# Kernel tuning notes

Hardware: AMD Instinct MI355X
Metric: run time of the kernel (lower is better)

The kernel has to match this reference:

```python
import jax, jax.numpy as jnp
import numpy as np

L, B, E = 512, 32, 512
ENC_HID, DEC_HID = 512, 1024
H2 = 2 * ENC_HID            # bidirectional encoder output dim
OUT_DIM = 32000             # generation (trg) vocab
CPY_LEN = 60000             # copy vocab size (embedding rows / prediction cols)
SRC_V = 50000
NEG = -1e10


def setup_inputs() -> dict:
    key = jax.random.key(0)
    ks = jax.random.split(key, 20)
    s = 0.02
    f32 = jnp.float32
    return {
        "src": jax.random.randint(ks[0], (L, B), 0, SRC_V),
        "inp": jax.random.randint(ks[1], (B,), 0, CPY_LEN),
        "hidden": jax.random.normal(ks[2], (2, B, DEC_HID), f32),
        "c": jax.random.normal(ks[3], (2, B, DEC_HID), f32),
        "encoder_outputs": jax.random.normal(ks[4], (L, B, H2), f32),
        "mask": jnp.ones((B, L), jnp.int32),
        "selective_weights": jax.random.normal(ks[5], (B, L - 2), f32),
        "src_to_cpy": jax.random.randint(ks[6], (SRC_V,), 0, CPY_LEN),
        # learned parameters
        "emb": jax.random.normal(ks[7], (CPY_LEN, E), f32) * s,
        "W_attn": jax.random.normal(ks[8], (H2 + DEC_HID, DEC_HID), f32) * s,
        "b_attn": jnp.zeros((DEC_HID,), f32),
        "v_attn": jax.random.normal(ks[9], (DEC_HID,), f32) * s,
        "W_ih0": jax.random.normal(ks[10], (4 * DEC_HID, 2 * H2 + E), f32) * s,
        "W_hh0": jax.random.normal(ks[11], (4 * DEC_HID, DEC_HID), f32) * s,
        "b_ih0": jnp.zeros((4 * DEC_HID,), f32),
        "b_hh0": jnp.zeros((4 * DEC_HID,), f32),
        "W_ih1": jax.random.normal(ks[12], (4 * DEC_HID, DEC_HID), f32) * s,
        "W_hh1": jax.random.normal(ks[13], (4 * DEC_HID, DEC_HID), f32) * s,
        "b_ih1": jnp.zeros((4 * DEC_HID,), f32),
        "b_hh1": jnp.zeros((4 * DEC_HID,), f32),
        "W_fc": jax.random.normal(ks[14], (OUT_DIM, H2 + DEC_HID + E), f32) * s,
        "b_fc": jnp.zeros((OUT_DIM,), f32),
        "W_copy": jax.random.normal(ks[15], (DEC_HID, H2), f32) * s,
        "b_copy": jnp.zeros((DEC_HID,), f32),
    }


def _lstm_cell(x, h, c, W_ih, W_hh, b_ih, b_hh):
    # PyTorch gate order: i, f, g, o
    g = x @ W_ih.T + h @ W_hh.T + b_ih + b_hh
    i, f, gg, o = jnp.split(g, 4, axis=-1)
    c_new = jax.nn.sigmoid(f) * c + jax.nn.sigmoid(i) * jnp.tanh(gg)
    h_new = jax.nn.sigmoid(o) * jnp.tanh(c_new)
    return h_new, c_new


def reference(src, inp, hidden, c, encoder_outputs, mask, selective_weights,
              src_to_cpy, emb, W_attn, b_attn, v_attn,
              W_ih0, W_hh0, b_ih0, b_hh0, W_ih1, W_hh1, b_ih1, b_hh1,
              W_fc, b_fc, W_copy, b_copy):
    Bn = encoder_outputs.shape[1]
    Ln = encoder_outputs.shape[0]
    # update_selective_weights: mask where converted src token != prev prediction, softmax
    conv_src = src_to_cpy[src[1:-1]]              # [L-2, B]
    copy_mask = (conv_src == inp[None, :]).T      # [B, L-2]
    sel = jnp.where(copy_mask, selective_weights, NEG)
    sel = jax.nn.softmax(sel, axis=1)             # [B, L-2]
    embedded = emb[inp]                           # [B, E] (dropout in eval mode = identity)
    enc = jnp.transpose(encoder_outputs, (1, 0, 2))  # [B, L, H2]
    # Bahdanau attention over encoder outputs
    h_top = hidden[-1]                            # [B, D]
    h_rep = jnp.broadcast_to(h_top[:, None, :], (Bn, Ln, h_top.shape[-1]))
    energy = jnp.tanh(jnp.concatenate([h_rep, enc], axis=2) @ W_attn + b_attn)  # [B, L, D]
    scores = energy @ v_attn                      # [B, L]
    scores = jnp.where(mask == 0, NEG, scores)
    attn_w = jax.nn.softmax(scores, axis=1)
    attentive_read = jnp.einsum('bl,blh->bh', attn_w, enc)        # [B, H2]
    sel = jnp.where(mask[:, 1:-1] == 0, NEG, sel)                 # faithful second mask
    selective_read = jnp.einsum('bl,blh->bh', sel, enc[:, 1:-1])  # [B, H2]
    # 2-layer LSTM, single step
    x = jnp.concatenate([embedded, attentive_read, selective_read], axis=1)
    h0, c0 = _lstm_cell(x, hidden[0], c[0], W_ih0, W_hh0, b_ih0, b_hh0)
    h1, c1 = _lstm_cell(h0, hidden[1], c[1], W_ih1, W_hh1, b_ih1, b_hh1)
    hidden_new = jnp.stack([h0, h1])
    c_new = jnp.stack([c0, c1])
    # generation scores
    gen = jnp.concatenate([h1, attentive_read, embedded], axis=1) @ W_fc.T + b_fc  # [B, OUT_DIM]
    # copy scores over trimmed source positions
    proj = jnp.tanh(enc[:, 1:-1] @ W_copy.T + b_copy)             # [B, L-2, D]
    copy_scores = jnp.einsum('bld,bd->bl', proj, h1)              # [B, L-2]
    copy_scores = jnp.where(mask[:, 1:-1] == 0, NEG, copy_scores)
    # assemble predictions: generation slice + indexed scatter of copy scores
    src_cpy = src_to_cpy[src.T[:, 1:-1]]                          # [B, L-2]
    preds = jnp.zeros((Bn, CPY_LEN), gen.dtype)
    preds = preds.at[:, :OUT_DIM].set(gen)
    preds = preds.at[jnp.arange(Bn)[:, None], src_cpy].set(copy_scores)
    return preds, hidden_new, c_new, attn_w, copy_scores
```

## Files before the change

kernel.cpp:

```cpp
#include <hip/hip_runtime.h>
#include <stdint.h>

typedef unsigned short u16;
typedef unsigned int   u32;
typedef __attribute__((ext_vector_type(8))) short short8;
typedef __attribute__((ext_vector_type(4))) float f32x4;

#define NEGF (-1.0e10f)

static constexpr int LL = 512, BB = 32, EE = 512, H2 = 1024, DH = 1024;
static constexpr int KX = 2560, OUTD = 32000, CPY = 60000;

static constexpr size_t HID_OFF   = 1920000;
static constexpr size_t C_OFF     = HID_OFF + 65536;
static constexpr size_t ATTN_OFF  = C_OFF + 65536;
static constexpr size_t CS_OFF    = ATTN_OFF + 16384;

static constexpr size_t WS_ENC    = 0;
static constexpr size_t WS_WA1T   = 33554432;
static constexpr size_t WS_WA2T   = 35651584;
static constexpr size_t WS_WCT    = 37748736;
static constexpr size_t WS_HPF    = 39845888;
static constexpr size_t WS_SCORES = 39976960;
static constexpr size_t WS_CSACC  = 40042496;
static constexpr size_t WS_SELP   = 40108032;
static constexpr size_t WS_XBF    = 40173568;
static constexpr size_t WS_GENBF  = 40337408;
static constexpr size_t WS_H0PBF  = 40501248;
static constexpr size_t WS_H1PBF  = 40566784;
static constexpr size_t WS_H0NBF  = 40632320;
static constexpr size_t WS_H1     = 41222144;
static constexpr size_t WS_TOTAL  = 41353216;
static constexpr size_t WS_GPART  = WS_WA1T;
static constexpr size_t WS_TAG    = WS_ENC;

__device__ __forceinline__ u16 f2bf(float x){
  u32 u = __builtin_bit_cast(u32, x);
  u32 r = (u + 0x7FFFu + ((u >> 16) & 1u)) >> 16;
  return (u16)r;
}
__device__ __forceinline__ float bf2f(u16 h){
  u32 u = ((u32)h) << 16; return __builtin_bit_cast(float, u);
}
__device__ __forceinline__ float fsig(float x){ return 1.f/(1.f + __expf(-x)); }
__device__ __forceinline__ float ftanh(float x){
  float e = __expf(2.f*x);
  return 1.f - 2.f/(e + 1.f);
}

#define GLDS16(gp, lp) __builtin_amdgcn_global_load_lds( \
    (__attribute__((address_space(1))) void*)(gp), \
    (__attribute__((address_space(3))) void*)(lp), 16, 0, 0)

__global__ void k_f32_to_bf16(const float* __restrict__ in, u16* __restrict__ out, int n4){
  int stride = gridDim.x * blockDim.x;
  for (int i = blockIdx.x*blockDim.x + threadIdx.x; i < n4; i += stride){
    float4 v = ((const float4*)in)[i];
    u32 lo = (u32)f2bf(v.x) | ((u32)f2bf(v.y) << 16);
    u32 hi = (u32)f2bf(v.z) | ((u32)f2bf(v.w) << 16);
    ((uint2*)out)[i] = make_uint2(lo, hi);
  }
}

__global__ void k_wattn_t(const float* __restrict__ W, u16* __restrict__ wa1t, u16* __restrict__ wa2t){
  __shared__ float Tt[64*65];
  int n0 = blockIdx.x*64, k0 = blockIdx.y*64;
  int t = threadIdx.x;
  int nn = t & 63, kq = t >> 6;
  for (int kk = kq; kk < 64; kk += 4)
    Tt[kk*65 + nn] = W[(size_t)(k0+kk)*1024 + n0 + nn];
  __syncthreads();
  u16* dst = (k0 < 1024) ? wa1t : wa2t;
  int kbase = (k0 < 1024) ? k0 : (k0 - 1024);
  int kk2 = t & 63, nq = t >> 6;
  for (int nn2 = nq; nn2 < 64; nn2 += 4)
    dst[(size_t)(n0+nn2)*1024 + kbase + kk2] = f2bf(Tt[kk2*65 + nn2]);
}

__global__ void k_prep(const int* __restrict__ src, const int* __restrict__ inp,
                       const float* __restrict__ hidden, const float* __restrict__ selw,
                       const int* __restrict__ s2c, const float* __restrict__ emb,
                       const int* __restrict__ mask,
                       u16* __restrict__ xbf, u16* __restrict__ genbf,
                       u16* __restrict__ h0pbf, u16* __restrict__ h1pbf,
                       float* __restrict__ scores, float* __restrict__ csacc,
                       float* __restrict__ selp)
{
  int b = blockIdx.x, t = threadIdx.x;
  int ib = inp[b];
  for (int h = t; h < 512; h += 256){
    u16 e = f2bf(emb[(size_t)ib*512 + h]);
    xbf[b*2560 + h] = e;
    genbf[b*2560 + 2048 + h] = e;
  }
  for (int k = t; k < 1024; k += 256){
    h0pbf[b*1024 + k] = f2bf(hidden[b*1024 + k]);
    h1pbf[b*1024 + k] = f2bf(hidden[32768 + b*1024 + k]);
  }
  for (int l = t; l < 512; l += 256){
    scores[b*512 + l] = 0.f;
    csacc[b*512 + l] = 0.f;
  }
  __shared__ float red[256];
  float lg[2];
  #pragma unroll
  for (int i = 0; i < 2; ++i){
    int j = t + i*256;
    lg[i] = NEGF;
    if (j < 510){
      int cs = s2c[src[(j+1)*32 + b]];
      if (cs == ib) lg[i] = selw[b*510 + j];
    }
  }
  red[t] = fmaxf(lg[0], lg[1]); __syncthreads();
  for (int s = 128; s > 0; s >>= 1){ if (t < s) red[t] = fmaxf(red[t], red[t+s]); __syncthreads(); }
  float mx = red[0]; __syncthreads();
  float e0 = (t < 510)     ? __expf(lg[0] - mx) : 0.f;
  float e1 = (t+256 < 510) ? __expf(lg[1] - mx) : 0.f;
  red[t] = e0 + e1; __syncthreads();
  for (int s = 128; s > 0; s >>= 1){ if (t < s) red[t] += red[t+s]; __syncthreads(); }
  float inv = 1.f / red[0];
  #pragma unroll
  for (int i = 0; i < 2; ++i){
    int j = t + i*256;
    if (j < 510){
      float v = ((i == 0) ? e0 : e1) * inv;
      int l = j + 1;
      selp[b*512 + l] = (mask[b*512 + l] != 0) ? v : NEGF;
    }
  }
}

__launch_bounds__(256)
__global__ void k_mfma(const u16* __restrict__ A, int lda, int Mvalid,
                       const u16* __restrict__ Bmat, int ldb, int K,
                       const float* __restrict__ preadd, int spa,
                       const float* __restrict__ dotw, int sdw,
                       float* __restrict__ dotout, int Ldot, int skipedge,
                       float* __restrict__ outstore, int NT)
{
  __shared__ u16 As[2][128*32];
  __shared__ u16 Bs[2][128*32];
  int nwg = gridDim.x, bid = blockIdx.x;
  int q = nwg >> 3, r = nwg & 7, xc = bid & 7, ix = bid >> 3;
  int wg = (xc < r ? xc*(q+1) : r*(q+1) + (xc - r)*q) + ix;
  int mt = wg / NT, nt = wg % NT;
  int m0 = mt * 128, n0 = nt * 128;
  int tid = threadIdx.x, lane = tid & 63, wid = tid >> 6;
  int wm = wid >> 1, wn = wid & 1;

  f32x4 acc[4][4];
  #pragma unroll
  for (int i = 0; i < 4; ++i)
    #pragma unroll
    for (int j = 0; j < 4; ++j)
      acc[i][j] = (f32x4){0.f, 0.f, 0.f, 0.f};

  int r0 = tid >> 2,          s0 = tid & 3;
  int r1 = (tid + 256) >> 2;
  int xv0 = (r0 ^ (r0 >> 2)) & 3, xv1 = (r1 ^ (r1 >> 2)) & 3;
  int sc0 = (s0 ^ xv0) << 3,      sc1 = (s0 ^ xv1) << 3;
  int raA0 = m0 + r0; if (raA0 >= Mvalid) raA0 = Mvalid - 1;
  int raA1 = m0 + r1; if (raA1 >= Mvalid) raA1 = Mvalid - 1;
  int rbB0 = n0 + r0, rbB1 = n0 + r1;

  auto stage = [&](int k0, u16* asb, u16* bsb){
    GLDS16(A    + (size_t)raA0*lda + k0 + sc0, (char*)asb + tid*16);
    GLDS16(A    + (size_t)raA1*lda + k0 + sc1, (char*)asb + (tid+256)*16);
    GLDS16(Bmat + (size_t)rbB0*ldb + k0 + sc0, (char*)bsb + tid*16);
    GLDS16(Bmat + (size_t)rbB1*ldb + k0 + sc1, (char*)bsb + (tid+256)*16);
  };

  int KT = K >> 5;
  stage(0, As[0], Bs[0]);
  for (int kt = 0; kt < KT; ++kt){
    __syncthreads();
    if (kt + 1 < KT) stage((kt+1) << 5, As[(kt+1) & 1], Bs[(kt+1) & 1]);
    const char* ap = (const char*)As[kt & 1];
    const char* bp = (const char*)Bs[kt & 1];
    short8 af[4], bfr[4];
    #pragma unroll
    for (int mi = 0; mi < 4; ++mi){
      int rr = wm*64 + mi*16 + (lane & 15);
      int xv = (rr ^ (rr >> 2)) & 3;
      af[mi] = *(const short8*)(ap + rr*64 + (((lane >> 4) ^ xv) << 4));
    }
    #pragma unroll
    for (int nj = 0; nj < 4; ++nj){
      int rr = wn*64 + nj*16 + (lane & 15);
      int xv = (rr ^ (rr >> 2)) & 3;
      bfr[nj] = *(const short8*)(bp + rr*64 + (((lane >> 4) ^ xv) << 4));
    }
    #pragma unroll
    for (int mi = 0; mi < 4; ++mi)
      #pragma unroll
      for (int nj = 0; nj < 4; ++nj)
        acc[mi][nj] = __builtin_amdgcn_mfma_f32_16x16x32_bf16(af[mi], bfr[nj], acc[mi][nj], 0, 0, 0);
  }

  int g = lane >> 4, cn = lane & 15;
  if (outstore){
    int Nld = NT * 128;
    #pragma unroll
    for (int mi = 0; mi < 4; ++mi)
      #pragma unroll
      for (int rr2 = 0; rr2 < 4; ++rr2){
        int row = m0 + wm*64 + mi*16 + g*4 + rr2;
        if (row < Mvalid){
          #pragma unroll
          for (int nj = 0; nj < 4; ++nj){
            int n = n0 + wn*64 + nj*16 + cn;
            outstore[(size_t)row*Nld + n] = acc[mi][nj][rr2] + preadd[(size_t)(row & 31)*spa + n];
          }
        }
      }
  } else {
    #pragma unroll
    for (int mi = 0; mi < 4; ++mi)
      #pragma unroll
      for (int rr2 = 0; rr2 < 4; ++rr2){
        int row = m0 + wm*64 + mi*16 + g*4 + rr2;
        int bb = row & 31;
        float part = 0.f;
        #pragma unroll
        for (int nj = 0; nj < 4; ++nj){
          int n = n0 + wn*64 + nj*16 + cn;
          float tv = ftanh(acc[mi][nj][rr2] + preadd[(size_t)bb*spa + n]);
          part = fmaf(tv, dotw[(size_t)bb*sdw + n], part);
        }
        part += __shfl_xor(part, 1);
        part += __shfl_xor(part, 2);
        part += __shfl_xor(part, 4);
        part += __shfl_xor(part, 8);
        if (cn == 0){
          int l = row >> 5;
          if (!skipedge || (l > 0 && l < Ldot - 1))
            atomicAdd(&dotout[(size_t)bb*Ldot + l], part);
        }
      }
  }
}

__global__ void k_softmax_attn(const float* __restrict__ scores, const int* __restrict__ mask,
                               float* __restrict__ attnw){
  int b = blockIdx.x, t = threadIdx.x;
  __shared__ float red[256];
  float v0 = scores[b*512 + t];
  float v1 = scores[b*512 + 256 + t];
  if (mask[b*512 + t] == 0) v0 = NEGF;
  if (mask[b*512 + 256 + t] == 0) v1 = NEGF;
  red[t] = fmaxf(v0, v1); __syncthreads();
  for (int s = 128; s > 0; s >>= 1){ if (t < s) red[t] = fmaxf(red[t], red[t+s]); __syncthreads(); }
  float mx = red[0]; __syncthreads();
  float e0 = __expf(v0 - mx), e1 = __expf(v1 - mx);
  red[t] = e0 + e1; __syncthreads();
  for (int s = 128; s > 0; s >>= 1){ if (t < s) red[t] += red[t+s]; __syncthreads(); }
  float inv = 1.f / red[0];
  attnw[b*512 + t] = e0 * inv;
  attnw[b*512 + 256 + t] = e1 * inv;
}

__global__ void k_reads(const u16* __restrict__ encbf, const float* __restrict__ attnw,
                        const float* __restrict__ selp,
                        u16* __restrict__ xbf, u16* __restrict__ genbf){
  int b = blockIdx.y;
  int tid = threadIdx.x;
  int h = blockIdx.x*256 + (tid & 255);
  int lh = tid >> 8;
  float aa = 0.f, as = 0.f;
  int l0 = lh*256, l1 = l0 + 256;
  #pragma unroll 4
  for (int l = l0; l < l1; ++l){
    float e = bf2f(encbf[((size_t)l*32 + b)*1024 + h]);
    aa = fmaf(attnw[b*512 + l], e, aa);
    if (l >= 1 && l < 511) as = fmaf(selp[b*512 + l], e, as);
  }
  __shared__ float red[512][2];
  red[tid][0] = aa; red[tid][1] = as;
  __syncthreads();
  if (tid < 256){
    aa = red[tid][0] + red[tid+256][0];
    as = red[tid][1] + red[tid+256][1];
    u16 ab = f2bf(aa);
    xbf[b*2560 + 512 + h]    = ab;
    xbf[b*2560 + 1536 + h]   = f2bf(as);
    genbf[b*2560 + 1024 + h] = ab;
  }
}

__launch_bounds__(256)
__global__ void k_wgemm(const float* __restrict__ W1, const u16* __restrict__ xb1, int K1,
                        const float* __restrict__ W2, const u16* __restrict__ xb2, int K2,
                        const float* __restrict__ bias1, const float* __restrict__ bias2,
                        float* __restrict__ outB, int ldo, int cps)
{
  __shared__ u16 As[64*64];
  __shared__ u16 Bs[2][32*64];
  const int tid = threadIdx.x, lane = tid & 63, w = tid >> 6;
  const int o0 = blockIdx.x * 64;
  const int c1 = K1 >> 6;
  const int c0 = blockIdx.y * cps;

  f32x4 acc[2];
  acc[0] = (f32x4){0.f,0.f,0.f,0.f};
  acc[1] = (f32x4){0.f,0.f,0.f,0.f};

  const int ar = tid >> 2, akq = (tid & 3) * 16;
  const int aswz = (ar & 7) << 4;
  const int brow = tid >> 3, pslot = tid & 7;
  const int lslot = pslot ^ (brow & 7);

  float4 aA[4], aB[4];

  auto aload = [&](int c, float4* dst){
    const float* Wp; int Kp, kc;
    if (c < c1){ Wp = W1; Kp = K1; kc = c << 6; }
    else       { Wp = W2; Kp = K2; kc = (c - c1) << 6; }
    const float4* p = (const float4*)(Wp + (size_t)(o0 + ar)*Kp + kc + akq);
    dst[0] = p[0]; dst[1] = p[1]; dst[2] = p[2]; dst[3] = p[3];
  };
  auto bstage = [&](int c, u16* bsb){
    const u16* xp; int Kp, kc;
    if (c < c1){ xp = xb1; Kp = K1; kc = c << 6; }
    else       { xp = xb2; Kp = K2; kc = (c - c1) << 6; }
    GLDS16(xp + (size_t)brow*Kp + kc + lslot*8, (char*)bsb + tid*16);
  };

  auto body = [&](int c, float4* cur, float4* nxt, const u16* bsCur, u16* bsNxt, bool more){
    __syncthreads();
    if (more){ aload(c + 1, nxt); bstage(c + 1, bsNxt); }
    u32 p0 = (u32)f2bf(cur[0].x) | ((u32)f2bf(cur[0].y) << 16);
    u32 p1 = (u32)f2bf(cur[0].z) | ((u32)f2bf(cur[0].w) << 16);
    u32 p2 = (u32)f2bf(cur[1].x) | ((u32)f2bf(cur[1].y) << 16);
    u32 p3 = (u32)f2bf(cur[1].z) | ((u32)f2bf(cur[1].w) << 16);
    u32 p4 = (u32)f2bf(cur[2].x) | ((u32)f2bf(cur[2].y) << 16);
    u32 p5 = (u32)f2bf(cur[2].z) | ((u32)f2bf(cur[2].w) << 16);
    u32 p6 = (u32)f2bf(cur[3].x) | ((u32)f2bf(cur[3].y) << 16);
    u32 p7 = (u32)f2bf(cur[3].z) | ((u32)f2bf(cur[3].w) << 16);
    char* rowp = (char*)As + ar*128;
    *(uint4*)(rowp + ((akq*2)      ^ aswz)) = make_uint4(p0,p1,p2,p3);
    *(uint4*)(rowp + ((akq*2 + 16) ^ aswz)) = make_uint4(p4,p5,p6,p7);
    asm volatile("s_waitcnt lgkmcnt(0)" ::: "memory");
    __builtin_amdgcn_s_barrier();
    #pragma unroll
    for (int kk = 0; kk < 2; ++kk){
      int rrA = w*16 + (lane & 15);
      int kb  = kk*64 + ((lane >> 4) << 4);
      short8 af = *(const short8*)((const char*)As + rrA*128 + (kb ^ ((rrA & 7) << 4)));
      #pragma unroll
      for (int nj = 0; nj < 2; ++nj){
        int rrB = nj*16 + (lane & 15);
        short8 bfv = *(const short8*)((const char*)bsCur + rrB*128 + (kb ^ ((rrB & 7) << 4)));
        acc[nj] = __builtin_amdgcn_mfma_f32_16x16x32_bf16(af, bfv, acc[nj], 0, 0, 0);
      }
    }
  };

  aload(c0, aA); bstage(c0, Bs[0]);
  for (int li = 0; li < cps; li += 2){
    body(c0 + li,     aA, aB, Bs[0], Bs[1], true);
    body(c0 + li + 1, aB, aA, Bs[1], Bs[0], (li + 2) < cps);
  }

  int g = lane >> 4, cn = lane & 15;
  int ob = o0 + w*16 + g*4;
  float* outP = outB + (size_t)blockIdx.y * 32 * (size_t)ldo;
  float4 badd = make_float4(0.f,0.f,0.f,0.f);
  if (blockIdx.y == 0){
    if (bias1){ float4 t = *(const float4*)(bias1 + ob);
      badd.x += t.x; badd.y += t.y; badd.z += t.z; badd.w += t.w; }
    if (bias2){ float4 t = *(const float4*)(bias2 + ob);
      badd.x += t.x; badd.y += t.y; badd.z += t.z; badd.w += t.w; }
  }
  #pragma unroll
  for (int nj = 0; nj < 2; ++nj){
    int bcol = nj*16 + cn;
    float4 v = make_float4(acc[nj][0] + badd.x, acc[nj][1] + badd.y,
                           acc[nj][2] + badd.z, acc[nj][3] + badd.w);
    *(float4*)(outP + (size_t)bcol*ldo + ob) = v;
  }
}

__global__ void k_cell(const float* __restrict__ gpart, const float* __restrict__ c_in,
                       float* __restrict__ h_out, float* __restrict__ c_out,
                       u16* __restrict__ hbf, int hld, float* __restrict__ h_plain){
  int idx = blockIdx.x*256 + threadIdx.x;
  int b = idx >> 10, j = idx & 1023;
  float gi = 0.f, gf = 0.f, gg = 0.f, go = 0.f;
  #pragma unroll
  for (int p = 0; p < 4; ++p){
    const float* gb = gpart + (size_t)p*131072 + (size_t)b*4096;
    gi += gb[j];
    gf += gb[1024 + j];
    gg += gb[2048 + j];
    go += gb[3072 + j];
  }
  float cv = c_in[b*1024 + j];
  float cnv = fsig(gf)*cv + fsig(gi)*ftanh(gg);
  float hn  = fsig(go)*ftanh(cnv);
  c_out[b*1024 + j] = cnv;
  h_out[b*1024 + j] = hn;
  hbf[(size_t)b*hld + j] = f2bf(hn);
  if (h_plain) h_plain[b*1024 + j] = hn;
}

__global__ void k_zerotail(float* __restrict__ preds){
  int i = blockIdx.x*256 + threadIdx.x;
  if (i < 224000){
    int b = i / 7000, t = i % 7000;
    ((float4*)(preds + (size_t)b*CPY + OUTD))[t] = make_float4(0.f, 0.f, 0.f, 0.f);
  }
}

__global__ void k_cstag(const float* __restrict__ csacc, const int* __restrict__ mask,
                        const int* __restrict__ src, const int* __restrict__ s2c,
                        float* __restrict__ cs_out, int* __restrict__ tag){
  int i = blockIdx.x*256 + threadIdx.x;
  if (i < 16320){
    int b = i / 510, j = i % 510, l = j + 1;
    cs_out[b*510 + j] = (mask[b*512 + l] != 0) ? csacc[b*512 + l] : NEGF;
    tag[(size_t)b*CPY + s2c[src[(j+1)*32 + b]]] = -1;
  }
}
__global__ void k_tag_max(const int* __restrict__ src, const int* __restrict__ s2c,
                          int* __restrict__ tag){
  int i = blockIdx.x*256 + threadIdx.x;
  if (i < 16320){
    int b = i / 510, j = i % 510;
    atomicMax(&tag[(size_t)b*CPY + s2c[src[(j+1)*32 + b]]], j);
  }
}
__global__ void k_tag_write(const int* __restrict__ src, const int* __restrict__ s2c,
                            const int* __restrict__ tag, const float* __restrict__ cs,
                            float* __restrict__ preds){
  int i = blockIdx.x*256 + threadIdx.x;
  if (i < 16320){
    int b = i / 510, j = i % 510;
    int idx = s2c[src[(j+1)*32 + b]];
    if (tag[(size_t)b*CPY + idx] == j)
      preds[(size_t)b*CPY + idx] = cs[b*510 + j];
  }
}

extern "C" void kernel_launch(void* const* d_in, const int* in_sizes, int n_in,
                              void* d_out, int out_size, void* d_ws, size_t ws_size,
                              hipStream_t stream){
  const int*   src    = (const int*)  d_in[0];
  const int*   inp    = (const int*)  d_in[1];
  const float* hidden = (const float*)d_in[2];
  const float* cst    = (const float*)d_in[3];
  const float* enc    = (const float*)d_in[4];
  const int*   mask   = (const int*)  d_in[5];
  const float* selw   = (const float*)d_in[6];
  const int*   s2c    = (const int*)  d_in[7];
  const float* emb    = (const float*)d_in[8];
  const float* W_attn = (const float*)d_in[9];
  const float* b_attn = (const float*)d_in[10];
  const float* v_attn = (const float*)d_in[11];
  const float* W_ih0  = (const float*)d_in[12];
  const float* W_hh0  = (const float*)d_in[13];
  const float* b_ih0  = (const float*)d_in[14];
  const float* b_hh0  = (const float*)d_in[15];
  const float* W_ih1  = (const float*)d_in[16];
  const float* W_hh1  = (const float*)d_in[17];
  const float* b_ih1  = (const float*)d_in[18];
  const float* b_hh1  = (const float*)d_in[19];
  const float* W_fc   = (const float*)d_in[20];
  const float* b_fc   = (const float*)d_in[21];
  const float* W_copy = (const float*)d_in[22];
  const float* b_copy = (const float*)d_in[23];

  if (ws_size < WS_TOTAL) return;

  float* out = (float*)d_out;
  char*  ws  = (char*)d_ws;
  u16*   encbf  = (u16*)  (ws + WS_ENC);
  u16*   wa1t   = (u16*)  (ws + WS_WA1T);
  u16*   wa2t   = (u16*)  (ws + WS_WA2T);
  u16*   wct    = (u16*)  (ws + WS_WCT);
  float* hpf    = (float*)(ws + WS_HPF);
  float* scores = (float*)(ws + WS_SCORES);
  float* csacc  = (float*)(ws + WS_CSACC);
  float* selp   = (float*)(ws + WS_SELP);
  u16*   xbf    = (u16*)  (ws + WS_XBF);
  u16*   genbf  = (u16*)  (ws + WS_GENBF);
  u16*   h0pbf  = (u16*)  (ws + WS_H0PBF);
  u16*   h1pbf  = (u16*)  (ws + WS_H1PBF);
  u16*   h0nbf  = (u16*)  (ws + WS_H0NBF);
  float* gpart  = (float*)(ws + WS_GPART);
  float* h1     = (float*)(ws + WS_H1);
  int*   tag    = (int*)  (ws + WS_TAG);

  k_f32_to_bf16<<<2048, 256, 0, stream>>>(enc,    encbf, (LL*BB*H2)/4);
  k_f32_to_bf16<<<512,  256, 0, stream>>>(W_copy, wct,   (DH*H2)/4);
  k_wattn_t<<<dim3(16, 32), 256, 0, stream>>>(W_attn, wa1t, wa2t);
  k_prep<<<32, 256, 0, stream>>>(src, inp, hidden, selw, s2c, emb, mask,
                                 xbf, genbf, h0pbf, h1pbf, scores, csacc, selp);

  k_mfma<<<8, 256, 0, stream>>>(h1pbf, 1024, 32, wa1t, 1024, 1024,
                                b_attn, 0, nullptr, 0, nullptr, 512, 0, hpf, 8);
  k_mfma<<<1024, 256, 0, stream>>>(encbf, 1024, LL*BB, wa2t, 1024, 1024,
                                   hpf, 1024, v_attn, 0, scores, 512, 0, nullptr, 8);
  k_softmax_attn<<<32, 256, 0, stream>>>(scores, mask, out + ATTN_OFF);
  k_reads<<<dim3(4, 32), 512, 0, stream>>>(encbf, out + ATTN_OFF, selp, xbf, genbf);

  k_wgemm<<<dim3(64, 4), 256, 0, stream>>>(W_ih0, xbf, KX, W_hh0, h0pbf, DH,
                                           b_ih0, b_hh0, gpart, 4096, 14);
  k_cell<<<128, 256, 0, stream>>>(gpart, cst, out + HID_OFF, out + C_OFF,
                                  h0nbf, 1024, nullptr);
  k_wgemm<<<dim3(64, 4), 256, 0, stream>>>(W_ih1, h0nbf, DH, W_hh1, h1pbf, DH,
                                           b_ih1, b_hh1, gpart, 4096, 8);
  k_cell<<<128, 256, 0, stream>>>(gpart, cst + 32768, out + HID_OFF + 32768,
                                  out + C_OFF + 32768, genbf, 2560, h1);

  k_mfma<<<1024, 256, 0, stream>>>(encbf, 1024, LL*BB, wct, 1024, 1024,
                                   b_copy, 0, h1, 1024, csacc, 512, 1, nullptr, 8);

  k_wgemm<<<dim3(500, 1), 256, 0, stream>>>(W_fc, genbf, KX, nullptr, nullptr, 0,
                                            b_fc, nullptr, out, CPY, 40);
  k_zerotail<<<875, 256, 0, stream>>>(out);

  k_cstag   <<<64, 256, 0, stream>>>(csacc, mask, src, s2c, out + CS_OFF, tag);
  k_tag_max <<<64, 256, 0, stream>>>(src, s2c, tag);
  k_tag_write<<<64, 256, 0, stream>>>(src, s2c, tag, out + CS_OFF, out);
}
```

Before: 395.6 us.

## Fuse attention and copy GEMMs over shared encoder tiles, defer copy dot

The attention-score GEMM and the copy-projection GEMM both read the bf16 encoder matrix, so they now run in one kernel that loads each A tile once and keeps two accumulator sets. The tanh'd copy projection is written to a 32 MB bf16 workspace and dotted with h1 later in a new per-row kernel that also writes copy scores and resets tags, which removes the separate cstag pass. The LSTM gate GEMMs also get more split-K partitions, with the cell kernel summing a variable number of partials. The cost is extra write and read traffic for the projection buffer, doubled register pressure in the fused kernel, and bf16 rounding of the projection before the dot.

```diff
diff --git a/kernel.cpp b/kernel.cpp
--- a/kernel.cpp
+++ b/kernel.cpp
@@ -22,15 +22,14 @@
 static constexpr size_t WS_WCT    = 37748736;
 static constexpr size_t WS_HPF    = 39845888;
 static constexpr size_t WS_SCORES = 39976960;
-static constexpr size_t WS_CSACC  = 40042496;
 static constexpr size_t WS_SELP   = 40108032;
 static constexpr size_t WS_XBF    = 40173568;
 static constexpr size_t WS_GENBF  = 40337408;
 static constexpr size_t WS_H0PBF  = 40501248;
 static constexpr size_t WS_H1PBF  = 40566784;
 static constexpr size_t WS_H0NBF  = 40632320;
-static constexpr size_t WS_H1     = 41222144;
-static constexpr size_t WS_TOTAL  = 41353216;
+static constexpr size_t WS_PROJ   = 50331648;
+static constexpr size_t WS_TOTAL  = WS_PROJ + 33554432;
 static constexpr size_t WS_GPART  = WS_WA1T;
 static constexpr size_t WS_TAG    = WS_ENC;
 
@@ -83,8 +82,7 @@
                        const int* __restrict__ mask,
                        u16* __restrict__ xbf, u16* __restrict__ genbf,
                        u16* __restrict__ h0pbf, u16* __restrict__ h1pbf,
-                       float* __restrict__ scores, float* __restrict__ csacc,
-                       float* __restrict__ selp)
+                       float* __restrict__ scores, float* __restrict__ selp)
 {
   int b = blockIdx.x, t = threadIdx.x;
   int ib = inp[b];
@@ -97,10 +95,8 @@
     h0pbf[b*1024 + k] = f2bf(hidden[b*1024 + k]);
     h1pbf[b*1024 + k] = f2bf(hidden[32768 + b*1024 + k]);
   }
-  for (int l = t; l < 512; l += 256){
+  for (int l = t; l < 512; l += 256)
     scores[b*512 + l] = 0.f;
-    csacc[b*512 + l] = 0.f;
-  }
   __shared__ float red[256];
   float lg[2];
   #pragma unroll
@@ -135,15 +131,11 @@
 __global__ void k_mfma(const u16* __restrict__ A, int lda, int Mvalid,
                        const u16* __restrict__ Bmat, int ldb, int K,
                        const float* __restrict__ preadd, int spa,
-                       const float* __restrict__ dotw, int sdw,
-                       float* __restrict__ dotout, int Ldot, int skipedge,
                        float* __restrict__ outstore, int NT)
 {
   __shared__ u16 As[2][128*32];
   __shared__ u16 Bs[2][128*32];
-  int nwg = gridDim.x, bid = blockIdx.x;
-  int q = nwg >> 3, r = nwg & 7, xc = bid & 7, ix = bid >> 3;
-  int wg = (xc < r ? xc*(q+1) : r*(q+1) + (xc - r)*q) + ix;
+  int wg = blockIdx.x;
   int mt = wg / NT, nt = wg % NT;
   int m0 = mt * 128, n0 = nt * 128;
   int tid = threadIdx.x, lane = tid & 63, wid = tid >> 6;
@@ -199,46 +191,134 @@
   }
 
   int g = lane >> 4, cn = lane & 15;
-  if (outstore){
-    int Nld = NT * 128;
-    #pragma unroll
-    for (int mi = 0; mi < 4; ++mi)
-      #pragma unroll
-      for (int rr2 = 0; rr2 < 4; ++rr2){
-        int row = m0 + wm*64 + mi*16 + g*4 + rr2;
-        if (row < Mvalid){
-          #pragma unroll
-          for (int nj = 0; nj < 4; ++nj){
-            int n = n0 + wn*64 + nj*16 + cn;
-            outstore[(size_t)row*Nld + n] = acc[mi][nj][rr2] + preadd[(size_t)(row & 31)*spa + n];
-          }
-        }
-      }
-  } else {
-    #pragma unroll
-    for (int mi = 0; mi < 4; ++mi)
-      #pragma unroll
-      for (int rr2 = 0; rr2 < 4; ++rr2){
-        int row = m0 + wm*64 + mi*16 + g*4 + rr2;
-        int bb = row & 31;
-        float part = 0.f;
+  int Nld = NT * 128;
+  #pragma unroll
+  for (int mi = 0; mi < 4; ++mi)
+    #pragma unroll
+    for (int rr2 = 0; rr2 < 4; ++rr2){
+      int row = m0 + wm*64 + mi*16 + g*4 + rr2;
+      if (row < Mvalid){
         #pragma unroll
         for (int nj = 0; nj < 4; ++nj){
           int n = n0 + wn*64 + nj*16 + cn;
-          float tv = ftanh(acc[mi][nj][rr2] + preadd[(size_t)bb*spa + n]);
-          part = fmaf(tv, dotw[(size_t)bb*sdw + n], part);
-        }
-        part += __shfl_xor(part, 1);
-        part += __shfl_xor(part, 2);
-        part += __shfl_xor(part, 4);
-        part += __shfl_xor(part, 8);
-        if (cn == 0){
-          int l = row >> 5;
-          if (!skipedge || (l > 0 && l < Ldot - 1))
-            atomicAdd(&dotout[(size_t)bb*Ldot + l], part);
+          outstore[(size_t)row*Nld + n] = acc[mi][nj][rr2] + preadd[(size_t)(row & 31)*spa + n];
         }
       }
-  }
+    }
+}
+
+__launch_bounds__(256, 2)
+__global__ void k_mfma2(const u16* __restrict__ A, const u16* __restrict__ B1,
+                        const u16* __restrict__ B2, const float* __restrict__ hpf,
+                        const float* __restrict__ vattn, const float* __restrict__ bcopy,
+                        float* __restrict__ scores, u16* __restrict__ projbf)
+{
+  __shared__ u16 As [2][128*32];
+  __shared__ u16 B1s[2][128*32];
+  __shared__ u16 B2s[2][128*32];
+  const int lda = 1024;
+  int nwg = gridDim.x, bid = blockIdx.x;
+  int q = nwg >> 3, r = nwg & 7, xc = bid & 7, ix = bid >> 3;
+  int wg = (xc < r ? xc*(q+1) : r*(q+1) + (xc - r)*q) + ix;
+  int mt = wg >> 3, nt = wg & 7;
+  int m0 = mt * 128, n0 = nt * 128;
+  int tid = threadIdx.x, lane = tid & 63, wid = tid >> 6;
+  int wm = wid >> 1, wn = wid & 1;
+
+  f32x4 acc1[4][4], acc2[4][4];
+  #pragma unroll
+  for (int i = 0; i < 4; ++i)
+    #pragma unroll
+    for (int j = 0; j < 4; ++j){
+      acc1[i][j] = (f32x4){0.f,0.f,0.f,0.f};
+      acc2[i][j] = (f32x4){0.f,0.f,0.f,0.f};
+    }
+
+  int r0 = tid >> 2,          s0 = tid & 3;
+  int r1 = (tid + 256) >> 2;
+  int xv0 = (r0 ^ (r0 >> 2)) & 3, xv1 = (r1 ^ (r1 >> 2)) & 3;
+  int sc0 = (s0 ^ xv0) << 3,      sc1 = (s0 ^ xv1) << 3;
+  size_t a0 = (size_t)(m0 + r0)*lda, a1 = (size_t)(m0 + r1)*lda;
+  size_t b0 = (size_t)(n0 + r0)*lda, b1o = (size_t)(n0 + r1)*lda;
+
+  auto stage = [&](int k0, int buf){
+    GLDS16(A  + a0  + k0 + sc0, (char*)As [buf] + tid*16);
+    GLDS16(A  + a1  + k0 + sc1, (char*)As [buf] + (tid+256)*16);
+    GLDS16(B1 + b0  + k0 + sc0, (char*)B1s[buf] + tid*16);
+    GLDS16(B1 + b1o + k0 + sc1, (char*)B1s[buf] + (tid+256)*16);
+    GLDS16(B2 + b0  + k0 + sc0, (char*)B2s[buf] + tid*16);
+    GLDS16(B2 + b1o + k0 + sc1, (char*)B2s[buf] + (tid+256)*16);
+  };
+
+  stage(0, 0);
+  for (int kt = 0; kt < 32; ++kt){
+    __syncthreads();
+    if (kt + 1 < 32) stage((kt+1) << 5, (kt+1) & 1);
+    const char* ap  = (const char*)As [kt & 1];
+    const char* b1p = (const char*)B1s[kt & 1];
+    const char* b2p = (const char*)B2s[kt & 1];
+    short8 af[4], bfr[4];
+    #pragma unroll
+    for (int mi = 0; mi < 4; ++mi){
+      int rr = wm*64 + mi*16 + (lane & 15);
+      int xv = (rr ^ (rr >> 2)) & 3;
+      af[mi] = *(const short8*)(ap + rr*64 + (((lane >> 4) ^ xv) << 4));
+    }
+    #pragma unroll
+    for (int nj = 0; nj < 4; ++nj){
+      int rr = wn*64 + nj*16 + (lane & 15);
+      int xv = (rr ^ (rr >> 2)) & 3;
+      bfr[nj] = *(const short8*)(b1p + rr*64 + (((lane >> 4) ^ xv) << 4));
+    }
+    #pragma unroll
+    for (int mi = 0; mi < 4; ++mi)
+      #pragma unroll
+      for (int nj = 0; nj < 4; ++nj)
+        acc1[mi][nj] = __builtin_amdgcn_mfma_f32_16x16x32_bf16(af[mi], bfr[nj], acc1[mi][nj], 0, 0, 0);
+    #pragma unroll
+    for (int nj = 0; nj < 4; ++nj){
+      int rr = wn*64 + nj*16 + (lane & 15);
+      int xv = (rr ^ (rr >> 2)) & 3;
+      bfr[nj] = *(const short8*)(b2p + rr*64 + (((lane >> 4) ^ xv) << 4));
+    }
+    #pragma unroll
+    for (int mi = 0; mi < 4; ++mi)
+      #pragma unroll
+      for (int nj = 0; nj < 4; ++nj)
+        acc2[mi][nj] = __builtin_amdgcn_mfma_f32_16x16x32_bf16(af[mi], bfr[nj], acc2[mi][nj], 0, 0, 0);
+  }
+
+  int g = lane >> 4, cn = lane & 15;
+  #pragma unroll
+  for (int mi = 0; mi < 4; ++mi)
+    #pragma unroll
+    for (int rr2 = 0; rr2 < 4; ++rr2){
+      int row = m0 + wm*64 + mi*16 + g*4 + rr2;
+      int bb = row & 31;
+      float part = 0.f;
+      #pragma unroll
+      for (int nj = 0; nj < 4; ++nj){
+        int n = n0 + wn*64 + nj*16 + cn;
+        float tv = ftanh(acc1[mi][nj][rr2] + hpf[(size_t)bb*1024 + n]);
+        part = fmaf(tv, vattn[n], part);
+      }
+      part += __shfl_xor(part, 1);
+      part += __shfl_xor(part, 2);
+      part += __shfl_xor(part, 4);
+      part += __shfl_xor(part, 8);
+      if (cn == 0) atomicAdd(&scores[(size_t)bb*512 + (row >> 5)], part);
+    }
+  #pragma unroll
+  for (int mi = 0; mi < 4; ++mi)
+    #pragma unroll
+    for (int rr2 = 0; rr2 < 4; ++rr2){
+      int row = m0 + wm*64 + mi*16 + g*4 + rr2;
+      #pragma unroll
+      for (int nj = 0; nj < 4; ++nj){
+        int n = n0 + wn*64 + nj*16 + cn;
+        projbf[(size_t)row*1024 + n] = f2bf(ftanh(acc2[mi][nj][rr2] + bcopy[n]));
+      }
+    }
 }
 
 __global__ void k_softmax_attn(const float* __restrict__ scores, const int* __restrict__ mask,
@@ -381,14 +461,14 @@
   }
 }
 
-__global__ void k_cell(const float* __restrict__ gpart, const float* __restrict__ c_in,
+__global__ void k_cell(const float* __restrict__ gpart, int nparts,
+                       const float* __restrict__ c_in,
                        float* __restrict__ h_out, float* __restrict__ c_out,
-                       u16* __restrict__ hbf, int hld, float* __restrict__ h_plain){
+                       u16* __restrict__ hbf, int hld){
   int idx = blockIdx.x*256 + threadIdx.x;
   int b = idx >> 10, j = idx & 1023;
   float gi = 0.f, gf = 0.f, gg = 0.f, go = 0.f;
-  #pragma unroll
-  for (int p = 0; p < 4; ++p){
+  for (int p = 0; p < nparts; ++p){
     const float* gb = gpart + (size_t)p*131072 + (size_t)b*4096;
     gi += gb[j];
     gf += gb[1024 + j];
@@ -401,7 +481,32 @@
   c_out[b*1024 + j] = cnv;
   h_out[b*1024 + j] = hn;
   hbf[(size_t)b*hld + j] = f2bf(hn);
-  if (h_plain) h_plain[b*1024 + j] = hn;
+}
+
+__global__ void k_pdot(const u16* __restrict__ projbf, const u16* __restrict__ genbf,
+                       const int* __restrict__ mask, const int* __restrict__ src,
+                       const int* __restrict__ s2c,
+                       float* __restrict__ cs_out, int* __restrict__ tag)
+{
+  int tid = threadIdx.x, lane = tid & 63, w = tid >> 6;
+  int row = blockIdx.x*4 + w;
+  int l = row >> 5, b = row & 31;
+  const u16* pr = projbf + (size_t)row*1024 + lane*16;
+  const u16* hr = genbf  + (size_t)b*2560 + lane*16;
+  short8 p0 = *(const short8*)pr,     p1 = *(const short8*)(pr + 8);
+  short8 h0 = *(const short8*)hr,     h1 = *(const short8*)(hr + 8);
+  float s = 0.f;
+  #pragma unroll
+  for (int i = 0; i < 8; ++i) s = fmaf(bf2f((u16)p0[i]), bf2f((u16)h0[i]), s);
+  #pragma unroll
+  for (int i = 0; i < 8; ++i) s = fmaf(bf2f((u16)p1[i]), bf2f((u16)h1[i]), s);
+  s += __shfl_xor(s, 1);  s += __shfl_xor(s, 2);  s += __shfl_xor(s, 4);
+  s += __shfl_xor(s, 8);  s += __shfl_xor(s, 16); s += __shfl_xor(s, 32);
+  if (lane == 0 && l >= 1 && l <= 510){
+    int j = l - 1;
+    cs_out[b*510 + j] = (mask[b*512 + l] != 0) ? s : NEGF;
+    tag[(size_t)b*CPY + s2c[src[l*32 + b]]] = -1;
+  }
 }
 
 __global__ void k_zerotail(float* __restrict__ preds){
@@ -412,16 +517,6 @@
   }
 }
 
-__global__ void k_cstag(const float* __restrict__ csacc, const int* __restrict__ mask,
-                        const int* __restrict__ src, const int* __restrict__ s2c,
-                        float* __restrict__ cs_out, int* __restrict__ tag){
-  int i = blockIdx.x*256 + threadIdx.x;
-  if (i < 16320){
-    int b = i / 510, j = i % 510, l = j + 1;
-    cs_out[b*510 + j] = (mask[b*512 + l] != 0) ? csacc[b*512 + l] : NEGF;
-    tag[(size_t)b*CPY + s2c[src[(j+1)*32 + b]]] = -1;
-  }
-}
 __global__ void k_tag_max(const int* __restrict__ src, const int* __restrict__ s2c,
                           int* __restrict__ tag){
   int i = blockIdx.x*256 + threadIdx.x;
@@ -480,47 +575,45 @@
   u16*   wct    = (u16*)  (ws + WS_WCT);
   float* hpf    = (float*)(ws + WS_HPF);
   float* scores = (float*)(ws + WS_SCORES);
-  float* csacc  = (float*)(ws + WS_CSACC);
   float* selp   = (float*)(ws + WS_SELP);
   u16*   xbf    = (u16*)  (ws + WS_XBF);
   u16*   genbf  = (u16*)  (ws + WS_GENBF);
   u16*   h0pbf  = (u16*)  (ws + WS_H0PBF);
   u16*   h1pbf  = (u16*)  (ws + WS_H1PBF);
   u16*   h0nbf  = (u16*)  (ws + WS_H0NBF);
+  u16*   projbf = (u16*)  (ws + WS_PROJ);
   float* gpart  = (float*)(ws + WS_GPART);
-  float* h1     = (float*)(ws + WS_H1);
   int*   tag    = (int*)  (ws + WS_TAG);
 
   k_f32_to_bf16<<<2048, 256, 0, stream>>>(enc,    encbf, (LL*BB*H2)/4);
   k_f32_to_bf16<<<512,  256, 0, stream>>>(W_copy, wct,   (DH*H2)/4);
   k_wattn_t<<<dim3(16, 32), 256, 0, stream>>>(W_attn, wa1t, wa2t);
   k_prep<<<32, 256, 0, stream>>>(src, inp, hidden, selw, s2c, emb, mask,
-                                 xbf, genbf, h0pbf, h1pbf, scores, csacc, selp);
+                                 xbf, genbf, h0pbf, h1pbf, scores, selp);
 
   k_mfma<<<8, 256, 0, stream>>>(h1pbf, 1024, 32, wa1t, 1024, 1024,
-                                b_attn, 0, nullptr, 0, nullptr, 512, 0, hpf, 8);
-  k_mfma<<<1024, 256, 0, stream>>>(encbf, 1024, LL*BB, wa2t, 1024, 1024,
-                                   hpf, 1024, v_attn, 0, scores, 512, 0, nullptr, 8);
+                                b_attn, 0, hpf, 8);
+  k_mfma2<<<1024, 256, 0, stream>>>(encbf, wa2t, wct, hpf, v_attn, b_copy,
+                                    scores, projbf);
   k_softmax_attn<<<32, 256, 0, stream>>>(scores, mask, out + ATTN_OFF);
   k_reads<<<dim3(4, 32), 512, 0, stream>>>(encbf, out + ATTN_OFF, selp, xbf, genbf);
 
-  k_wgemm<<<dim3(64, 4), 256, 0, stream>>>(W_ih0, xbf, KX, W_hh0, h0pbf, DH,
-                                           b_ih0, b_hh0, gpart, 4096, 14);
-  k_cell<<<128, 256, 0, stream>>>(gpart, cst, out + HID_OFF, out + C_OFF,
-                                  h0nbf, 1024, nullptr);
-  k_wgemm<<<dim3(64, 4), 256, 0, stream>>>(W_ih1, h0nbf, DH, W_hh1, h1pbf, DH,
-                                           b_ih1, b_hh1, gpart, 4096, 8);
-  k_cell<<<128, 256, 0, stream>>>(gpart, cst + 32768, out + HID_OFF + 32768,
-                                  out + C_OFF + 32768, genbf, 2560, h1);
-
-  k_mfma<<<1024, 256, 0, stream>>>(encbf, 1024, LL*BB, wct, 1024, 1024,
-                                   b_copy, 0, h1, 1024, csacc, 512, 1, nullptr, 8);
+  k_wgemm<<<dim3(64, 7), 256, 0, stream>>>(W_ih0, xbf, KX, W_hh0, h0pbf, DH,
+                                           b_ih0, b_hh0, gpart, 4096, 8);
+  k_cell<<<128, 256, 0, stream>>>(gpart, 7, cst, out + HID_OFF, out + C_OFF,
+                                  h0nbf, 1024);
+  k_wgemm<<<dim3(64, 8), 256, 0, stream>>>(W_ih1, h0nbf, DH, W_hh1, h1pbf, DH,
+                                           b_ih1, b_hh1, gpart, 4096, 4);
+  k_cell<<<128, 256, 0, stream>>>(gpart, 8, cst + 32768, out + HID_OFF + 32768,
+                                  out + C_OFF + 32768, genbf, 2560);
+
+  k_pdot<<<4096, 256, 0, stream>>>(projbf, genbf, mask, src, s2c,
+                                   out + CS_OFF, tag);
 
   k_wgemm<<<dim3(500, 1), 256, 0, stream>>>(W_fc, genbf, KX, nullptr, nullptr, 0,
                                             b_fc, nullptr, out, CPY, 40);
   k_zerotail<<<875, 256, 0, stream>>>(out);
 
-  k_cstag   <<<64, 256, 0, stream>>>(csacc, mask, src, s2c, out + CS_OFF, tag);
-  k_tag_max <<<64, 256, 0, stream>>>(src, s2c, tag);
+  k_tag_max  <<<64, 256, 0, stream>>>(src, s2c, tag);
   k_tag_write<<<64, 256, 0, stream>>>(src, s2c, tag, out + CS_OFF, out);
 }
```

Result: faster. 378.8 us (-4.3%).
